# Kernel tuning notes

Hardware: AMD Instinct MI355X
Metric: run time of the kernel (lower is better)

## Reference

```python
import jax, jax.numpy as jnp
import numpy as np

B, E = 256, 512
C, K = 8192, 10          # n_class, n_center
LMD = 10.0
INV_GAMMA = 10.0         # 1 / gamma, gamma = 0.1
TAU = 0.2
MARGIN = 0.01


def setup_inputs() -> dict:
    key = jax.random.key(0)
    k1, k2, k3 = jax.random.split(key, 3)
    embeddings = jax.random.normal(k1, (B, E), dtype=jnp.float32)
    labels = jax.random.randint(k2, (B,), 0, C, dtype=jnp.int64)
    fc = jax.random.normal(k3, (C * K, E), dtype=jnp.float32)
    return {"embeddings": embeddings, "labels": labels, "fc": fc}


def reference(embeddings, labels, fc):
    # L2-normalize centers (rows of fc), like F.normalize(fc, p=2, dim=1)
    norm = jnp.sqrt(jnp.sum(fc * fc, axis=1, keepdims=True))
    w = fc / jnp.maximum(norm, 1e-12)

    # similarity to every center: [B, C, K]
    x = (embeddings @ w.T).reshape(B, C, K)
    prob = jax.nn.softmax(INV_GAMMA * x, axis=2)
    h = jnp.sum(prob * x, axis=2)  # [B, C] soft-pooled class similarity

    # subtract margin on ground-truth class, then cross-entropy
    rows = jnp.arange(B)
    margin_m = jnp.zeros_like(h).at[rows, labels].set(MARGIN)
    logits = LMD * (h - margin_m)
    logp = jax.nn.log_softmax(logits, axis=1)
    loss_cls = -jnp.mean(logp[rows, labels])

    # regularizer: batched per-class center gram, replaces python loop over C
    wc = w.reshape(C, K, E)
    sub = 1.0 - jnp.einsum('cke,cje->ckj', wc, wc)   # [C, K, K]
    sub = jnp.where(sub <= 0.0, 1e-10, sub)
    mask = jnp.triu(jnp.ones((K, K), dtype=bool), k=1)  # strict upper triangle
    safe = jnp.where(mask, 2.0 * sub, 1.0)
    reg = jnp.sum(jnp.where(mask, jnp.sqrt(safe), 0.0))
    reg = reg / (C * K * (K - 1.0))
    return loss_cls + TAU * reg
```

## Files before the change

kernel.cpp:

```cpp
#include <hip/hip_runtime.h>


typedef __bf16 bf16;
typedef bf16 bf16x8 __attribute__((ext_vector_type(8)));
typedef float f32x4 __attribute__((ext_vector_type(4)));

#define NCLASS 8192
#define KC 10
#define EDIM 512
#define BATCH 256
#define BK 64

__device__ inline void load_lds16(const void* g, void* l) {
    __builtin_amdgcn_global_load_lds(
        (const __attribute__((address_space(1))) void*)g,
        (__attribute__((address_space(3))) void*)l, 16, 0, 0);
}

__global__ __launch_bounds__(256) void prep_kernel(
    const float* __restrict__ fc, bf16* __restrict__ w,
    float* __restrict__ gram_part,
    const float* __restrict__ e, bf16* __restrict__ At)
{
    __shared__ float rows[KC * EDIM];
    __shared__ float s_invn[KC];
    __shared__ float s_wsum[4];
    const int t = threadIdx.x;

    if (blockIdx.x >= NCLASS) {
        int i = (blockIdx.x - NCLASS) * 256 + t;
        int row = i >> 6, chunk = i & 63;
        int k = chunk * 8;
        float4 a = ((const float4*)e)[i * 2];
        float4 b = ((const float4*)e)[i * 2 + 1];
        bf16x8 v;
        v[0] = (bf16)a.x; v[1] = (bf16)a.y; v[2] = (bf16)a.z; v[3] = (bf16)a.w;
        v[4] = (bf16)b.x; v[5] = (bf16)b.y; v[6] = (bf16)b.z; v[7] = (bf16)b.w;
        *(bf16x8*)&At[((k >> 5) << 13) + (row << 5) + (k & 31)] = v;
        return;
    }

    const int c = blockIdx.x;
    const int wave = t >> 6, lane = t & 63;

    const float4* src = (const float4*)(fc + (size_t)c * (KC * EDIM));
    float4* rows4 = (float4*)rows;
    #pragma unroll
    for (int i = 0; i < 5; ++i) rows4[t + i * 256] = src[t + i * 256];
    __syncthreads();

    for (int r = wave; r < KC; r += 4) {
        float s = 0.f;
        #pragma unroll
        for (int j = 0; j < 8; ++j) {
            float v = rows[r * EDIM + lane + j * 64];
            s += v * v;
        }
        #pragma unroll
        for (int off = 32; off; off >>= 1) s += __shfl_xor(s, off);
        if (lane == 0) s_invn[r] = 1.0f / fmaxf(sqrtf(s), 1e-12f);
    }
    __syncthreads();

    bf16x8* dst = (bf16x8*)(w + (size_t)c * (KC * EDIM));
    #pragma unroll
    for (int p = 0; p < 3; ++p) {
        int j = t + p * 256;
        if (j < 640) {
            int r = j >> 6;
            float inv = s_invn[r];
            float4 a = *(const float4*)(rows + j * 8);
            float4 b = *(const float4*)(rows + j * 8 + 4);
            bf16x8 v;
            v[0] = (bf16)(a.x * inv); v[1] = (bf16)(a.y * inv);
            v[2] = (bf16)(a.z * inv); v[3] = (bf16)(a.w * inv);
            v[4] = (bf16)(b.x * inv); v[5] = (bf16)(b.y * inv);
            v[6] = (bf16)(b.z * inv); v[7] = (bf16)(b.w * inv);
            dst[j] = v;
        }
    }

    float part = 0.f;
    for (int p = wave; p < 45; p += 4) {
        int i = 0, pp = p;
        while (pp >= 9 - i) { pp -= 9 - i; ++i; }
        int j = i + 1 + pp;
        float s = 0.f;
        #pragma unroll
        for (int u = 0; u < 8; ++u)
            s += rows[i * EDIM + lane + u * 64] * rows[j * EDIM + lane + u * 64];
        #pragma unroll
        for (int off = 32; off; off >>= 1) s += __shfl_xor(s, off);
        if (lane == 0) {
            float sub = 1.0f - s * s_invn[i] * s_invn[j];
            if (sub <= 0.0f) sub = 1e-10f;
            part += sqrtf(2.0f * sub);
        }
    }
    if (lane == 0) s_wsum[wave] = part;
    __syncthreads();
    if (t == 0) gram_part[c] = s_wsum[0] + s_wsum[1] + s_wsum[2] + s_wsum[3];
}

__global__ __launch_bounds__(512, 2) void gemm_h_kernel(
    const bf16* __restrict__ W,
    const bf16* __restrict__ At,
    float* __restrict__ h)
{
    __shared__ bf16 Ws[2][80 * BK];
    const int tid = threadIdx.x;
    const int wave = tid >> 6, lane = tid & 63;

    f32x4 acc[5][2];
    #pragma unroll
    for (int mt = 0; mt < 5; ++mt)
        #pragma unroll
        for (int nt = 0; nt < 2; ++nt)
            acc[mt][nt] = (f32x4){0.f, 0.f, 0.f, 0.f};

    const size_t g0 = (size_t)blockIdx.x * 80;

    const int rA = tid >> 3, sA = tid & 7;
    const bf16* srcA = W + (g0 + rA) * EDIM + ((sA ^ (rA & 7)) << 3);
    const int rB = (512 + tid) >> 3, sB = tid & 7;
    const bf16* srcB = W + (g0 + rB) * EDIM + ((sB ^ (rB & 7)) << 3);

    const int q = lane >> 4;
    const int q8 = q * 8;
    const int fr = lane & 15;

    load_lds16(srcA, &Ws[0][wave * 512]);
    if (tid < 128) load_lds16(srcB, &Ws[0][4096 + wave * 512]);
    __syncthreads();

    for (int t = 0; t < 8; ++t) {
        const int cur = t & 1;
        if (t < 7) {
            const int kb = (t + 1) * BK;
            load_lds16(srcA + kb, &Ws[cur ^ 1][wave * 512]);
            if (tid < 128) load_lds16(srcB + kb, &Ws[cur ^ 1][4096 + wave * 512]);
        }
        #pragma unroll
        for (int kk = 0; kk < BK; kk += 32) {
            const int ccb = kk >> 3;
            bf16x8 wf[5], ef[2];
            #pragma unroll
            for (int nt = 0; nt < 2; ++nt) {
                int row = wave * 32 + nt * 16 + fr;
                ef[nt] = *(const bf16x8*)
                    &At[((t * 2 + (kk >> 5)) << 13) + (row << 5) + q8];
            }
            #pragma unroll
            for (int mt = 0; mt < 5; ++mt) {
                int row = mt * 16 + fr;
                int s = (ccb + q) ^ (row & 7);
                wf[mt] = *(const bf16x8*)&Ws[cur][row * BK + (s << 3)];
            }
            #pragma unroll
            for (int mt = 0; mt < 5; ++mt)
                #pragma unroll
                for (int nt = 0; nt < 2; ++nt)
                    acc[mt][nt] = __builtin_amdgcn_mfma_f32_16x16x32_bf16(
                        wf[mt], ef[nt], acc[mt][nt], 0, 0, 0);
        }
        __syncthreads();
    }

    const int col = lane & 15;
    const int quad = lane >> 4;
    const int cb = blockIdx.x * 8;
    #pragma unroll
    for (int nt = 0; nt < 2; ++nt) {
        int b = wave * 32 + nt * 16 + col;
        float hval[8];
        #pragma unroll
        for (int cc = 0; cc < 8; ++cc) {
            float xm = -1e30f;
            #pragma unroll
            for (int mt = 0; mt < 5; ++mt) {
                if (10 * cc + 10 > 16 * mt && 10 * cc < 16 * mt + 16) {
                    #pragma unroll
                    for (int rg = 0; rg < 4; ++rg) {
                        int r = 16 * mt + 4 * quad + rg;
                        if (r >= 10 * cc && r < 10 * cc + 10)
                            xm = fmaxf(xm, acc[mt][nt][rg]);
                    }
                }
            }
            xm = fmaxf(xm, __shfl_xor(xm, 16));
            xm = fmaxf(xm, __shfl_xor(xm, 32));
            float s1 = 0.f, s2 = 0.f;
            #pragma unroll
            for (int mt = 0; mt < 5; ++mt) {
                if (10 * cc + 10 > 16 * mt && 10 * cc < 16 * mt + 16) {
                    #pragma unroll
                    for (int rg = 0; rg < 4; ++rg) {
                        int r = 16 * mt + 4 * quad + rg;
                        if (r >= 10 * cc && r < 10 * cc + 10) {
                            float x = acc[mt][nt][rg];
                            float e = __expf(10.0f * (x - xm));
                            s1 += e; s2 += e * x;
                        }
                    }
                }
            }
            s1 += __shfl_xor(s1, 16); s1 += __shfl_xor(s1, 32);
            s2 += __shfl_xor(s2, 16); s2 += __shfl_xor(s2, 32);
            hval[cc] = s2 / s1;
        }
        if (quad == 0) {
            float4 v0 = {hval[0], hval[1], hval[2], hval[3]};
            float4 v1 = {hval[4], hval[5], hval[6], hval[7]};
            float4* dst = (float4*)&h[(size_t)b * NCLASS + cb];
            dst[0] = v0;
            dst[1] = v1;
        }
    }
}

__global__ __launch_bounds__(256) void ce_kernel(
    const float* __restrict__ h, const int* __restrict__ labels,
    float* __restrict__ ce_part)
{
    __shared__ float redm[4];
    __shared__ float reds[4];
    const int b = blockIdx.x, t = threadIdx.x;
    const int wave = t >> 6, lane = t & 63;
    const int lbl = labels[b];
    const float* hb = h + (size_t)b * NCLASS;
    const float4* hb4 = (const float4*)hb;
    const int lq = lbl >> 2, lr = lbl & 3;

    float4 v[8];
    float mx = -1e30f;
    #pragma unroll
    for (int k = 0; k < 8; ++k) {
        int idx = t + k * 256;
        float4 x = hb4[idx];
        x.x = 10.0f * x.x - ((idx == lq && lr == 0) ? 0.1f : 0.0f);
        x.y = 10.0f * x.y - ((idx == lq && lr == 1) ? 0.1f : 0.0f);
        x.z = 10.0f * x.z - ((idx == lq && lr == 2) ? 0.1f : 0.0f);
        x.w = 10.0f * x.w - ((idx == lq && lr == 3) ? 0.1f : 0.0f);
        v[k] = x;
        mx = fmaxf(mx, fmaxf(fmaxf(x.x, x.y), fmaxf(x.z, x.w)));
    }
    #pragma unroll
    for (int off = 32; off; off >>= 1) mx = fmaxf(mx, __shfl_xor(mx, off));
    if (lane == 0) redm[wave] = mx;
    __syncthreads();
    mx = fmaxf(fmaxf(redm[0], redm[1]), fmaxf(redm[2], redm[3]));

    float s = 0.f;
    #pragma unroll
    for (int k = 0; k < 8; ++k) {
        s += __expf(v[k].x - mx) + __expf(v[k].y - mx)
           + __expf(v[k].z - mx) + __expf(v[k].w - mx);
    }
    #pragma unroll
    for (int off = 32; off; off >>= 1) s += __shfl_xor(s, off);
    if (lane == 0) reds[wave] = s;
    __syncthreads();
    if (t == 0) {
        s = reds[0] + reds[1] + reds[2] + reds[3];
        float logit_l = 10.0f * (hb[lbl] - 0.01f);
        ce_part[b] = mx + logf(s) - logit_l;
    }
}

__global__ __launch_bounds__(256) void final_kernel(
    const float* __restrict__ gram_part, const float* __restrict__ ce_part,
    float* __restrict__ out)
{
    __shared__ float red[4];
    const int t = threadIdx.x, wave = t >> 6, lane = t & 63;
    const float4* gp4 = (const float4*)gram_part;
    float g = 0.f;
    #pragma unroll
    for (int i = 0; i < 8; ++i) {
        float4 x = gp4[t + i * 256];
        g += x.x + x.y + x.z + x.w;
    }
    float val = ce_part[t] * (1.0f / 256.0f)
              + g * (0.2f / 737280.0f);
    #pragma unroll
    for (int off = 32; off; off >>= 1) val += __shfl_xor(val, off);
    if (lane == 0) red[wave] = val;
    __syncthreads();
    if (t == 0) out[0] = red[0] + red[1] + red[2] + red[3];
}

extern "C" void kernel_launch(void* const* d_in, const int* in_sizes, int n_in,
                              void* d_out, int out_size, void* d_ws, size_t ws_size,
                              hipStream_t stream) {
    const float* emb    = (const float*)d_in[0];
    const int*   labels = (const int*)d_in[1];
    const float* fc     = (const float*)d_in[2];
    float* out = (float*)d_out;

    char* ws = (char*)d_ws;
    bf16*  w         = (bf16*)ws;
    bf16*  At        = (bf16*)(ws + 83886080);
    float* h         = (float*)(ws + 84148352);
    float* gram_part = (float*)(ws + 92536960);
    float* ce_part   = (float*)(ws + 92569728);

    prep_kernel<<<NCLASS + 64, 256, 0, stream>>>(fc, w, gram_part, emb, At);
    gemm_h_kernel<<<81920 / 80, 512, 0, stream>>>(w, At, h);
    ce_kernel<<<BATCH, 256, 0, stream>>>(h, labels, ce_part);
    final_kernel<<<1, 256, 0, stream>>>(gram_part, ce_part, out);
}
```

Baseline: 300.2 us.

## Fuse cross-entropy sum-exp into GEMM epilogue with atomics, drop ce kernel

The GEMM epilogue no longer writes the full [B, C] h matrix. It now computes exp(10*h) per class directly, subtracting the margin for the label class. It also records the label logit and atomically accumulates a per-row sum of exponentials into a buffer that an extra prep block zeroes. The separate cross-entropy kernel and the 8 MB h round-trip are removed, and the final kernel takes the log of the sum. Dropping max subtraction relies on logits being bounded by roughly ±10. The atomics add contention on 256 addresses and make the summation order nondeterministic.

```diff
diff --git a/kernel.cpp b/kernel.cpp
--- a/kernel.cpp
+++ b/kernel.cpp
@@ -20,7 +20,8 @@
 __global__ __launch_bounds__(256) void prep_kernel(
     const float* __restrict__ fc, bf16* __restrict__ w,
     float* __restrict__ gram_part,
-    const float* __restrict__ e, bf16* __restrict__ At)
+    const float* __restrict__ e, bf16* __restrict__ At,
+    float* __restrict__ sumexp)
 {
     __shared__ float rows[KC * EDIM];
     __shared__ float s_invn[KC];
@@ -28,6 +29,10 @@
     const int t = threadIdx.x;
 
     if (blockIdx.x >= NCLASS) {
+        if (blockIdx.x == NCLASS + 64) {
+            sumexp[t] = 0.0f;
+            return;
+        }
         int i = (blockIdx.x - NCLASS) * 256 + t;
         int row = i >> 6, chunk = i & 63;
         int k = chunk * 8;
@@ -105,7 +110,9 @@
 __global__ __launch_bounds__(512, 2) void gemm_h_kernel(
     const bf16* __restrict__ W,
     const bf16* __restrict__ At,
-    float* __restrict__ h)
+    const int* __restrict__ labels,
+    float* __restrict__ sumexp,
+    float* __restrict__ lab_logit)
 {
     __shared__ bf16 Ws[2][80 * BK];
     const int tid = threadIdx.x;
@@ -209,67 +216,25 @@
             hval[cc] = s2 / s1;
         }
         if (quad == 0) {
-            float4 v0 = {hval[0], hval[1], hval[2], hval[3]};
-            float4 v1 = {hval[4], hval[5], hval[6], hval[7]};
-            float4* dst = (float4*)&h[(size_t)b * NCLASS + cb];
-            dst[0] = v0;
-            dst[1] = v1;
-        }
-    }
-}
-
-__global__ __launch_bounds__(256) void ce_kernel(
-    const float* __restrict__ h, const int* __restrict__ labels,
-    float* __restrict__ ce_part)
-{
-    __shared__ float redm[4];
-    __shared__ float reds[4];
-    const int b = blockIdx.x, t = threadIdx.x;
-    const int wave = t >> 6, lane = t & 63;
-    const int lbl = labels[b];
-    const float* hb = h + (size_t)b * NCLASS;
-    const float4* hb4 = (const float4*)hb;
-    const int lq = lbl >> 2, lr = lbl & 3;
-
-    float4 v[8];
-    float mx = -1e30f;
-    #pragma unroll
-    for (int k = 0; k < 8; ++k) {
-        int idx = t + k * 256;
-        float4 x = hb4[idx];
-        x.x = 10.0f * x.x - ((idx == lq && lr == 0) ? 0.1f : 0.0f);
-        x.y = 10.0f * x.y - ((idx == lq && lr == 1) ? 0.1f : 0.0f);
-        x.z = 10.0f * x.z - ((idx == lq && lr == 2) ? 0.1f : 0.0f);
-        x.w = 10.0f * x.w - ((idx == lq && lr == 3) ? 0.1f : 0.0f);
-        v[k] = x;
-        mx = fmaxf(mx, fmaxf(fmaxf(x.x, x.y), fmaxf(x.z, x.w)));
-    }
-    #pragma unroll
-    for (int off = 32; off; off >>= 1) mx = fmaxf(mx, __shfl_xor(mx, off));
-    if (lane == 0) redm[wave] = mx;
-    __syncthreads();
-    mx = fmaxf(fmaxf(redm[0], redm[1]), fmaxf(redm[2], redm[3]));
-
-    float s = 0.f;
-    #pragma unroll
-    for (int k = 0; k < 8; ++k) {
-        s += __expf(v[k].x - mx) + __expf(v[k].y - mx)
-           + __expf(v[k].z - mx) + __expf(v[k].w - mx);
-    }
-    #pragma unroll
-    for (int off = 32; off; off >>= 1) s += __shfl_xor(s, off);
-    if (lane == 0) reds[wave] = s;
-    __syncthreads();
-    if (t == 0) {
-        s = reds[0] + reds[1] + reds[2] + reds[3];
-        float logit_l = 10.0f * (hb[lbl] - 0.01f);
-        ce_part[b] = mx + logf(s) - logit_l;
+            const int lbl = labels[b];
+            float ps = 0.f;
+            #pragma unroll
+            for (int cc = 0; cc < 8; ++cc) {
+                float lg = 10.0f * hval[cc];
+                if (lbl == cb + cc) {
+                    lg -= 0.1f;
+                    lab_logit[b] = lg;
+                }
+                ps += __expf(lg);
+            }
+            atomicAdd(&sumexp[b], ps);
+        }
     }
 }
 
 __global__ __launch_bounds__(256) void final_kernel(
-    const float* __restrict__ gram_part, const float* __restrict__ ce_part,
-    float* __restrict__ out)
+    const float* __restrict__ gram_part, const float* __restrict__ sumexp,
+    const float* __restrict__ lab_logit, float* __restrict__ out)
 {
     __shared__ float red[4];
     const int t = threadIdx.x, wave = t >> 6, lane = t & 63;
@@ -280,7 +245,8 @@
         float4 x = gp4[t + i * 256];
         g += x.x + x.y + x.z + x.w;
     }
-    float val = ce_part[t] * (1.0f / 256.0f)
+    float ce = logf(sumexp[t]) - lab_logit[t];
+    float val = ce * (1.0f / 256.0f)
               + g * (0.2f / 737280.0f);
     #pragma unroll
     for (int off = 32; off; off >>= 1) val += __shfl_xor(val, off);
@@ -300,12 +266,13 @@
     char* ws = (char*)d_ws;
     bf16*  w         = (bf16*)ws;
     bf16*  At        = (bf16*)(ws + 83886080);
-    float* h         = (float*)(ws + 84148352);
-    float* gram_part = (float*)(ws + 92536960);
-    float* ce_part   = (float*)(ws + 92569728);
-
-    prep_kernel<<<NCLASS + 64, 256, 0, stream>>>(fc, w, gram_part, emb, At);
-    gemm_h_kernel<<<81920 / 80, 512, 0, stream>>>(w, At, h);
-    ce_kernel<<<BATCH, 256, 0, stream>>>(h, labels, ce_part);
-    final_kernel<<<1, 256, 0, stream>>>(gram_part, ce_part, out);
-}
+    float* gram_part = (float*)(ws + 84148224);
+    float* sumexp    = (float*)(ws + 84181248);
+    float* lab_logit = (float*)(ws + 84182272);
+
+    prep_kernel<<<NCLASS + 65, 256, 0, stream>>>(fc, w, gram_part, emb, At,
+                                                 sumexp);
+    gemm_h_kernel<<<81920 / 80, 512, 0, stream>>>(w, At, labels,
+                                                  sumexp, lab_logit);
+    final_kernel<<<1, 256, 0, stream>>>(gram_part, sumexp, lab_logit, out);
+}
```

Result: no change. 304.6 us (+1.4%).
